# Performance work log

Measured on AMD Instinct MI355X. Metric: run time of the kernel, lower is better.

The kernel has to match this reference:

```python
import jax, jax.numpy as jnp
import numpy as np


def setup_inputs() -> dict:
    key = jax.random.key(0)
    k1, k2 = jax.random.split(key)
    B, N, M, D = 4, 8192, 8192, 3
    pred_points = jax.random.normal(k1, (B, N, D), dtype=jnp.float32)
    gt_points = jax.random.normal(k2, (B, M, D), dtype=jnp.float32)
    return {"pred_points": pred_points, "gt_points": gt_points}


def reference(pred_points, gt_points):
    p2 = jnp.sum(pred_points * pred_points, axis=-1)  # [B, N]
    g2 = jnp.sum(gt_points * gt_points, axis=-1)      # [B, M]
    cross = jnp.einsum("bnd,bmd->bnm", pred_points, gt_points)  # [B, N, M]
    d2 = p2[:, :, None] + g2[:, None, :] - 2.0 * cross
    dist = jnp.sqrt(jnp.maximum(d2, 0.0))             # [B, N, M]
    min_pred_to_gt = jnp.min(dist, axis=-1)           # [B, N]
    min_gt_to_pred = jnp.min(dist, axis=-2)           # [B, M]
    return min_pred_to_gt.mean() + min_gt_to_pred.mean()
```

## Files before the change

### kernel.cpp

```cpp
#include <hip/hip_runtime.h>


#define B_ 4
#define N_ 8192
#define THREADS 512

typedef float f32x16 __attribute__((ext_vector_type(16)));
typedef short short8 __attribute__((ext_vector_type(8)));
typedef unsigned short ushort8 __attribute__((ext_vector_type(8)));

__device__ __forceinline__ unsigned short f2bf(float x) {
  unsigned u = __float_as_uint(x);
  u = u + 0x7FFFu + ((u >> 16) & 1u);
  return (unsigned short)(u >> 16);
}
__device__ __forceinline__ float bf2f(unsigned short h) {
  return __uint_as_float(((unsigned)h) << 16);
}

__global__ __launch_bounds__(256) void chamfer_pack(
    const float* __restrict__ pred, const float* __restrict__ gt,
    unsigned short* __restrict__ Apack, unsigned short* __restrict__ Bpack,
    float* __restrict__ accws) {
  const int i = blockIdx.x * 256 + threadIdx.x;
  if (i < 2) ((unsigned*)accws)[i] = 0u;
  const int half = B_ * N_;
  const float* src = (i < half) ? pred : gt;
  const int k = (i < half) ? i : i - half;
  const float x = src[3 * k], y = src[3 * k + 1], z = src[3 * k + 2];
  const float q2 = fmaf(x, x, fmaf(y, y, z * z));

  const float ux = -2.f * x, uy = -2.f * y, uz = -2.f * z;
  const unsigned short uhx = f2bf(ux), uhy = f2bf(uy), uhz = f2bf(uz);
  const unsigned short ulx = f2bf(ux - bf2f(uhx));
  const unsigned short uly = f2bf(uy - bf2f(uhy));
  const unsigned short ulz = f2bf(uz - bf2f(uhz));
  const unsigned short thx = f2bf(x), thy = f2bf(y), thz = f2bf(z);
  const unsigned short tlx = f2bf(x - bf2f(thx));
  const unsigned short tly = f2bf(y - bf2f(thy));
  const unsigned short tlz = f2bf(z - bf2f(thz));
  const unsigned short q2h = f2bf(q2);
  const unsigned short q2l = f2bf(q2 - bf2f(q2h));
  const unsigned short one = 0x3F80u;

  const size_t aslot = (size_t)i;
  const size_t bslot = (size_t)((i < half) ? i + half : i - half);

  ushort8 alo = {uhx, uhy, uhz, uhx, uhy, uhz, ulx, uly};
  ushort8 ahi = {ulz, q2h, q2l, one, one, 0, 0, 0};
  ushort8 blo = {thx, thy, thz, tlx, tly, tlz, thx, thy};
  ushort8 bhi = {thz, one, one, q2h, q2l, 0, 0, 0};
  *(ushort8*)(Apack + aslot * 16) = alo;
  *(ushort8*)(Apack + aslot * 16 + 8) = ahi;
  *(ushort8*)(Bpack + bslot * 16) = blo;
  *(ushort8*)(Bpack + bslot * 16 + 8) = bhi;
}

__global__ __launch_bounds__(THREADS, 4) void chamfer_mfma(
    const unsigned short* __restrict__ Apack,
    const unsigned short* __restrict__ Bpack,
    float* __restrict__ rowmin) {
  __shared__ unsigned rowlds[64];
  const int tid = threadIdx.x;
  const int dirb = blockIdx.y;
  const int panel = blockIdx.x;
  const int w = tid >> 6, l = tid & 63;
  const int wr = w >> 2, wc = w & 3;
  const int l31 = l & 31, lhi = l >> 5;

  if (tid < 64) rowlds[tid] = 0x7F7FFFFFu;
  __syncthreads();

  const int row = panel * 64 + wr * 32 + l31;
  const short8 afrag =
      *(const short8*)(Apack + ((size_t)dirb * N_ + row) * 16 + lhi * 8);

  const unsigned short* bp =
      Bpack + ((size_t)dirb * N_ + wc * 32 + l31) * 16 + lhi * 8;

  const f32x16 zacc = {};
  float racc[16];
#pragma unroll
  for (int r = 0; r < 16; ++r) racc[r] = 3.4e38f;

#pragma unroll 2
  for (int step = 0; step < 64; ++step) {
    const short8 bfrag = *(const short8*)(bp + (size_t)step * 128 * 16);
    const f32x16 d =
        __builtin_amdgcn_mfma_f32_32x32x16_bf16(afrag, bfrag, zacc, 0, 0, 0);
#pragma unroll
    for (int r = 0; r < 16; ++r) racc[r] = fminf(racc[r], d[r]);
  }

#pragma unroll
  for (int r = 0; r < 16; ++r) racc[r] = fmaxf(racc[r], 0.0f);
#pragma unroll
  for (int m = 1; m <= 16; m <<= 1)
#pragma unroll
    for (int r = 0; r < 16; ++r)
      racc[r] = fminf(racc[r], __shfl_xor(racc[r], m, 64));

  if (l31 == 0) {
#pragma unroll
    for (int r = 0; r < 16; ++r) {
      const int lr = wr * 32 + (r & 3) + 8 * (r >> 2) + 4 * lhi;
      atomicMin(&rowlds[lr], __float_as_uint(racc[r]));
    }
  }
  __syncthreads();
  if (tid < 64)
    rowmin[(size_t)dirb * N_ + panel * 64 + tid] = __uint_as_float(rowlds[tid]);
}

__global__ __launch_bounds__(256) void chamfer_fin(
    const float* __restrict__ rowmin, float* __restrict__ accws,
    float* __restrict__ out) {
  const int t = blockIdx.x * 256 + threadIdx.x;
  const float4 v = ((const float4*)rowmin)[t];
  float sum = sqrtf(fmaxf(v.x, 0.f)) + sqrtf(fmaxf(v.y, 0.f)) +
              sqrtf(fmaxf(v.z, 0.f)) + sqrtf(fmaxf(v.w, 0.f));
#pragma unroll
  for (int off = 32; off > 0; off >>= 1) sum += __shfl_down(sum, off, 64);
  __shared__ float ws4[4];
  const int lane = threadIdx.x & 63, wid = threadIdx.x >> 6;
  if (lane == 0) ws4[wid] = sum;
  __syncthreads();
  if (threadIdx.x == 0) {
    const float bs = (ws4[0] + ws4[1]) + (ws4[2] + ws4[3]);
    atomicAdd(&accws[0], bs);
    __threadfence();
    const unsigned old = atomicAdd(((unsigned*)accws) + 1, 1u);
    if (old == gridDim.x - 1) {
      __threadfence();
      const float tot = atomicAdd(&accws[0], 0.0f);
      out[0] = tot * (1.0f / 32768.0f);
    }
  }
}

extern "C" void kernel_launch(void* const* d_in, const int* in_sizes, int n_in,
                              void* d_out, int out_size, void* d_ws, size_t ws_size,
                              hipStream_t stream) {
  const float* pred = (const float*)d_in[0];
  const float* gt   = (const float*)d_in[1];
  float* out = (float*)d_out;

  float* accws = (float*)d_ws;
  unsigned short* Apack = (unsigned short*)((char*)d_ws + 64);
  unsigned short* Bpack = Apack + (size_t)2 * B_ * N_ * 16;
  float* rowmin = (float*)(Bpack + (size_t)2 * B_ * N_ * 16);

  chamfer_pack<<<256, 256, 0, stream>>>(pred, gt, Apack, Bpack, accws);
  chamfer_mfma<<<dim3(128, 8), THREADS, 0, stream>>>(Apack, Bpack, rowmin);
  chamfer_fin<<<64, 256, 0, stream>>>(rowmin, accws, out);
}
```

Baseline: 87.60 us.

## Stage B tiles through double-buffered LDS and compute two row tiles per wave

B-operand fragments are now staged into shared memory in 512-column chunks using asynchronous global-to-LDS loads with double buffering. Each wave now covers all 64 rows of the panel, issuing two MFMAs per B fragment so each fragment is reused across two A tiles. This is meant to replace repeated scattered global loads of B with coalesced shared staging and to hide load latency. In exchange it adds 32 KB of LDS per block, a block-wide barrier per chunk and doubled accumulator registers, which may reduce occupancy.

```diff
diff --git a/kernel.cpp b/kernel.cpp
--- a/kernel.cpp
+++ b/kernel.cpp
@@ -4,6 +4,8 @@
 #define B_ 4
 #define N_ 8192
 #define THREADS 512
+#define CHUNK_COLS 512
+#define NCHUNK (N_ / CHUNK_COLS)
 
 typedef float f32x16 __attribute__((ext_vector_type(16)));
 typedef short short8 __attribute__((ext_vector_type(8)));
@@ -56,55 +58,94 @@
   *(ushort8*)(Bpack + bslot * 16 + 8) = bhi;
 }
 
+__device__ __forceinline__ void stage_chunk(
+    const unsigned short* __restrict__ Bdir, int chunk,
+    unsigned short* ldsbase, int w, int l) {
+  const unsigned short* g =
+      Bdir + (size_t)chunk * CHUNK_COLS * 16 + (size_t)(w * 64) * 16 + l * 8;
+  unsigned short* d = ldsbase + (w * 64) * 16;
+#pragma unroll
+  for (int k = 0; k < 2; ++k) {
+    __builtin_amdgcn_global_load_lds(
+        (const __attribute__((address_space(1))) unsigned int*)(g + k * 512),
+        (__attribute__((address_space(3))) unsigned int*)(d + k * 512),
+        16, 0, 0);
+  }
+}
+
 __global__ __launch_bounds__(THREADS, 4) void chamfer_mfma(
     const unsigned short* __restrict__ Apack,
     const unsigned short* __restrict__ Bpack,
     float* __restrict__ rowmin) {
+  __shared__ unsigned short buf[2][CHUNK_COLS * 16];
   __shared__ unsigned rowlds[64];
+
   const int tid = threadIdx.x;
   const int dirb = blockIdx.y;
   const int panel = blockIdx.x;
   const int w = tid >> 6, l = tid & 63;
-  const int wr = w >> 2, wc = w & 3;
   const int l31 = l & 31, lhi = l >> 5;
 
   if (tid < 64) rowlds[tid] = 0x7F7FFFFFu;
+
+  const size_t abase = ((size_t)dirb * N_ + panel * 64) * 16;
+  const short8 afrag0 = *(const short8*)(Apack + abase + (size_t)l31 * 16 + lhi * 8);
+  const short8 afrag1 = *(const short8*)(Apack + abase + (size_t)(32 + l31) * 16 + lhi * 8);
+
+  const unsigned short* Bdir = Bpack + (size_t)dirb * N_ * 16;
+
+  stage_chunk(Bdir, 0, &buf[0][0], w, l);
+
+  const f32x16 zacc = {};
+  float racc0[16], racc1[16];
+#pragma unroll
+  for (int r = 0; r < 16; ++r) { racc0[r] = 3.4e38f; racc1[r] = 3.4e38f; }
+
   __syncthreads();
 
-  const int row = panel * 64 + wr * 32 + l31;
-  const short8 afrag =
-      *(const short8*)(Apack + ((size_t)dirb * N_ + row) * 16 + lhi * 8);
+  for (int c = 0; c < NCHUNK; ++c) {
+    const int cur = c & 1;
+    if (c + 1 < NCHUNK)
+      stage_chunk(Bdir, c + 1, &buf[cur ^ 1][0], w, l);
 
-  const unsigned short* bp =
-      Bpack + ((size_t)dirb * N_ + wc * 32 + l31) * 16 + lhi * 8;
-
-  const f32x16 zacc = {};
-  float racc[16];
+    const unsigned short* bb = &buf[cur][0];
 #pragma unroll
-  for (int r = 0; r < 16; ++r) racc[r] = 3.4e38f;
-
-#pragma unroll 2
-  for (int step = 0; step < 64; ++step) {
-    const short8 bfrag = *(const short8*)(bp + (size_t)step * 128 * 16);
-    const f32x16 d =
-        __builtin_amdgcn_mfma_f32_32x32x16_bf16(afrag, bfrag, zacc, 0, 0, 0);
+    for (int sub = 0; sub < 2; ++sub) {
+      const int col = w * 64 + sub * 32 + l31;
+      const short8 bfrag = *(const short8*)(bb + (size_t)col * 16 + lhi * 8);
+      const f32x16 d0 =
+          __builtin_amdgcn_mfma_f32_32x32x16_bf16(afrag0, bfrag, zacc, 0, 0, 0);
+      const f32x16 d1 =
+          __builtin_amdgcn_mfma_f32_32x32x16_bf16(afrag1, bfrag, zacc, 0, 0, 0);
 #pragma unroll
-    for (int r = 0; r < 16; ++r) racc[r] = fminf(racc[r], d[r]);
+      for (int r = 0; r < 16; ++r) {
+        racc0[r] = fminf(racc0[r], d0[r]);
+        racc1[r] = fminf(racc1[r], d1[r]);
+      }
+    }
+    __syncthreads();
   }
 
 #pragma unroll
-  for (int r = 0; r < 16; ++r) racc[r] = fmaxf(racc[r], 0.0f);
+  for (int r = 0; r < 16; ++r) {
+    racc0[r] = fmaxf(racc0[r], 0.0f);
+    racc1[r] = fmaxf(racc1[r], 0.0f);
+  }
 #pragma unroll
-  for (int m = 1; m <= 16; m <<= 1)
+  for (int m = 1; m <= 16; m <<= 1) {
 #pragma unroll
-    for (int r = 0; r < 16; ++r)
-      racc[r] = fminf(racc[r], __shfl_xor(racc[r], m, 64));
+    for (int r = 0; r < 16; ++r) {
+      racc0[r] = fminf(racc0[r], __shfl_xor(racc0[r], m, 64));
+      racc1[r] = fminf(racc1[r], __shfl_xor(racc1[r], m, 64));
+    }
+  }
 
   if (l31 == 0) {
 #pragma unroll
     for (int r = 0; r < 16; ++r) {
-      const int lr = wr * 32 + (r & 3) + 8 * (r >> 2) + 4 * lhi;
-      atomicMin(&rowlds[lr], __float_as_uint(racc[r]));
+      const int lr = (r & 3) + 8 * (r >> 2) + 4 * lhi;
+      atomicMin(&rowlds[lr], __float_as_uint(racc0[r]));
+      atomicMin(&rowlds[32 + lr], __float_as_uint(racc1[r]));
     }
   }
   __syncthreads();
```

Result: slower. 97.11 us (+10.9%).
